# Kernel optimization log

Hardware: AMD Instinct MI355X
Metric: run time of the kernel (lower is better)

Reference implementation:

```python
import jax, jax.numpy as jnp
import numpy as np

N_V, M, K, C, H, F, CO = 100000, 25000, 48, 64, 4, 256, 64


def setup_inputs() -> dict:
    key = jax.random.key(0)
    ks = jax.random.split(key, 16)
    w = lambda k, shape: (jax.random.normal(k, shape, jnp.float32) * 0.05)
    voxel_features = jax.random.normal(ks[0], (N_V, C), jnp.float32)
    voxel_coords = jax.random.uniform(ks[1], (N_V, 3), jnp.float32) * 70.0 - 35.0
    query_coords = jax.random.uniform(ks[2], (M, 3), jnp.float32) * 70.0 - 35.0
    key_indices = jax.random.randint(ks[3], (M, K), 0, N_V, jnp.int32)
    key_mask = jax.random.uniform(ks[4], (M, K)) < 0.3
    key_mask = key_mask.at[:, 0].set(False)  # guarantee >=1 valid key per query
    zeros = lambda n: jnp.zeros((n,), jnp.float32)
    ones = lambda n: jnp.ones((n,), jnp.float32)
    return dict(
        voxel_features=voxel_features, voxel_coords=voxel_coords,
        query_coords=query_coords, key_indices=key_indices, key_mask=key_mask,
        q_pos_w=w(ks[5], (C, 3)), q_pos_b=zeros(C),
        k_pos_w=w(ks[6], (C, 3)), k_pos_b=zeros(C),
        in_proj_w=w(ks[7], (3 * C, C)), in_proj_b=zeros(3 * C),
        out_proj_w=w(ks[8], (C, C)), out_proj_b=zeros(C),
        lin1_w=w(ks[9], (F, C)), lin1_b=zeros(F),
        lin2_w=w(ks[10], (C, F)), lin2_b=zeros(C),
        norm_g=ones(C), norm_b=zeros(C), norm_m=zeros(C), norm_v=ones(C),
        out_w=w(ks[11], (CO, C)), out_b=zeros(CO),
        bn2_g=ones(CO), bn2_b=zeros(CO), bn2_m=zeros(CO), bn2_v=ones(CO),
    )


def reference(voxel_features, voxel_coords, query_coords, key_indices, key_mask,
              q_pos_w, q_pos_b, k_pos_w, k_pos_b, in_proj_w, in_proj_b,
              out_proj_w, out_proj_b, lin1_w, lin1_b, lin2_w, lin2_b,
              norm_g, norm_b, norm_m, norm_v, out_w, out_b,
              bn2_g, bn2_b, bn2_m, bn2_v):
    m, k = key_indices.shape
    c = voxel_features.shape[1]
    h = H
    d = c // h
    # grouping_operation: gather per-query key features/coords  (M,K,C)/(M,K,3)
    key_feats = voxel_features[key_indices]
    rel = voxel_coords[key_indices] - query_coords[:, None, :]  # relative coords
    # k_pos_proj: Conv1d(3->C, kernel 1) + ReLU == pointwise linear
    key_pos = jax.nn.relu(jnp.einsum('mkt,ct->mkc', rel, k_pos_w) + k_pos_b)
    k_in = key_feats + key_pos                      # (M,K,C)
    # q_pos_proj: Linear(3->C) + ReLU
    q_in = jax.nn.relu(query_coords @ q_pos_w.T + q_pos_b)  # (M,C)
    # nn.MultiheadAttention, query len 1, batch = M, keys = K
    wq, wk, wv = jnp.split(in_proj_w, 3, axis=0)
    bq, bk, bv = jnp.split(in_proj_b, 3)
    q = ((q_in @ wq.T + bq) * (d ** -0.5)).reshape(m, h, d)
    kk = (k_in @ wk.T + bk).reshape(m, k, h, d)
    vv = (k_in @ wv.T + bv).reshape(m, k, h, d)
    s = jnp.einsum('mhd,mkhd->mhk', q, kk)
    s = jnp.where(key_mask[:, None, :], -1e9, s)    # key_padding_mask
    a = jax.nn.softmax(s, axis=-1)
    o = jnp.einsum('mhk,mkhd->mhd', a, vv).reshape(m, c)
    attend = o @ out_proj_w.T + out_proj_b          # (M,C)
    # FFN residual (dropouts are identity in eval)
    ff = jax.nn.relu(attend @ lin1_w.T + lin1_b) @ lin2_w.T + lin2_b
    x = attend + ff
    # BatchNorm1d (eval)
    x = (x - norm_m) / jnp.sqrt(norm_v + 1e-5) * norm_g + norm_b
    # output_layer: Linear -> BN -> ReLU
    y = x @ out_w.T + out_b
    y = (y - bn2_m) / jnp.sqrt(bn2_v + 1e-5) * bn2_g + bn2_b
    return jax.nn.relu(y)
```

## Files before the change

### kernel.cpp

```cpp
#include <hip/hip_runtime.h>
#include <math.h>

#define CC 64
#define KK 48
#define HH 4

typedef __attribute__((ext_vector_type(8))) short s16x8;
typedef __attribute__((ext_vector_type(4))) short s16x4;
typedef __attribute__((ext_vector_type(4))) float f32x4;

#define QW_OFF_U16 57344

#define WAVEFENCE() asm volatile("s_waitcnt lgkmcnt(0)" ::: "memory")

__device__ __forceinline__ unsigned short f2bf(float f) {
  return (unsigned short)((__float_as_uint(f) + 0x8000u) >> 16);
}
__device__ __forceinline__ float bf2f(unsigned short h) {
  return __uint_as_float(((unsigned)h) << 16);
}

__global__ __launch_bounds__(256) void prep_kernel(
    const float* __restrict__ ipw, const float* __restrict__ opw,
    const float* __restrict__ l1w, const float* __restrict__ l2w,
    const float* __restrict__ ow,
    const float* __restrict__ ng, const float* __restrict__ nb,
    const float* __restrict__ nm, const float* __restrict__ nv,
    const float* __restrict__ b2g, const float* __restrict__ b2b,
    const float* __restrict__ b2m, const float* __restrict__ b2v,
    const unsigned char* __restrict__ km,
    float* __restrict__ ws)
{
  unsigned short* wsu = (unsigned short*)ws;
  if (blockIdx.x == 209) {
    int any = 0;
    for (int i = threadIdx.x; i < 4096; i += 256)
      if ((i & 3) && km[i]) any = 1;
    __shared__ int sb;
    if (threadIdx.x == 0) sb = 0;
    __syncthreads();
    if (any) atomicOr(&sb, 1);
    __syncthreads();
    if (threadIdx.x == 0) ((int*)ws)[26880] = sb;
    return;
  }
  int e = blockIdx.x * 256 + threadIdx.x;
  if (e < 4096)        wsu[e] = f2bf(ipw[e]);
  else if (e < 8192)  { int i = e - 4096; int h = i >> 10, c = (i >> 4) & 63, d = i & 15;
                        wsu[e] = f2bf(ipw[(size_t)(64 + h * 16 + d) * 64 + c]); }
  else if (e < 12288)  wsu[e] = f2bf(ipw[e]);
  else if (e < 16384)  wsu[e] = f2bf(opw[e - 12288]);
  else if (e < 32768)  wsu[e] = f2bf(l1w[e - 16384]);
  else if (e < 49152)  wsu[e] = f2bf(l2w[e - 32768]);
  else if (e < 53248)  wsu[e] = f2bf(ow[e - 49152]);
  else if (e < 53312) { int c = e - 53248; float s = ng[c] / sqrtf(nv[c] + 1e-5f);
                        ws[26624 + c] = s; ws[26624 + 64 + c] = nb[c] - nm[c] * s; }
  else if (e < 53376) { int c = e - 53312; float s = b2g[c] / sqrtf(b2v[c] + 1e-5f);
                        ws[26752 + c] = s; ws[26752 + 64 + c] = b2b[c] - b2m[c] * s; }
}

__global__ __launch_bounds__(256) void castv_kernel(
    const float* __restrict__ vf, const float* __restrict__ vcoord,
    unsigned short* __restrict__ vfb, float4* __restrict__ vc4, int NV)
{
  const int i0 = blockIdx.x * 256 + threadIdx.x;
  const int stride = gridDim.x * 256;
  for (int i = i0; i < NV * 16; i += stride) {
    const float4 v = *(const float4*)(vf + (size_t)i * 4);
    s16x4 p; p[0] = (short)f2bf(v.x); p[1] = (short)f2bf(v.y);
    p[2] = (short)f2bf(v.z); p[3] = (short)f2bf(v.w);
    *(s16x4*)(vfb + (size_t)i * 4) = p;
  }
  for (int i = i0; i < NV; i += stride)
    vc4[i] = make_float4(vcoord[i * 3], vcoord[i * 3 + 1], vcoord[i * 3 + 2], 0.f);
}

__global__ __launch_bounds__(256, 2) void qprep_kernel(
    const float* __restrict__ qcoord, const float* __restrict__ qpw,
    const float* __restrict__ qpb, const float* __restrict__ ipb,
    const unsigned short* __restrict__ wq_bf,
    const unsigned short* __restrict__ wk2T_bf,
    unsigned short* __restrict__ qw_out, int M)
{
  __shared__ __align__(16) unsigned short xa[4][1024];
  __shared__ float qc[4][48];
  const int w = threadIdx.x >> 6, l = threadIdx.x & 63;
  const int col = l & 15, lg = l >> 4;
  const int r0 = blockIdx.x * 64 + w * 16;

  if (l < 48) {
    int gi = r0 * 3 + l;
    qc[w][l] = (gi < M * 3) ? qcoord[gi] : 0.f;
  }
  const int c0 = col * 4;
  const float4 wA = *(const float4*)(qpw + c0 * 3);
  const float4 wB = *(const float4*)(qpw + c0 * 3 + 4);
  const float4 wC = *(const float4*)(qpw + c0 * 3 + 8);
  const float4 bq4 = *(const float4*)(qpb + c0);
  __syncthreads();

  #pragma unroll
  for (int i = 0; i < 4; ++i) {
    const int row = i * 4 + lg;
    const float x = qc[w][row * 3 + 0], y = qc[w][row * 3 + 1], z = qc[w][row * 3 + 2];
    s16x4 p;
    p[0] = (short)f2bf(fmaxf(wA.x * x + wA.y * y + wA.z * z + bq4.x, 0.f));
    p[1] = (short)f2bf(fmaxf(wA.w * x + wB.x * y + wB.y * z + bq4.y, 0.f));
    p[2] = (short)f2bf(fmaxf(wB.z * x + wB.w * y + wC.x * z + bq4.z, 0.f));
    p[3] = (short)f2bf(fmaxf(wC.y * x + wC.z * y + wC.w * z + bq4.w, 0.f));
    *(s16x4*)&xa[w][(row * 64 + c0) ^ ((row & 7) << 3)] = p;
  }
  __syncthreads();

  {
    s16x8 af0 = *(const s16x8*)&xa[w][(col * 64 + 0 + lg * 8) ^ ((col & 7) << 3)];
    s16x8 af1 = *(const s16x8*)&xa[w][(col * 64 + 32 + lg * 8) ^ ((col & 7) << 3)];
    f32x4 qv[4];
    #pragma unroll
    for (int nt = 0; nt < 4; ++nt) {
      f32x4 acc = {0.f, 0.f, 0.f, 0.f};
      acc = __builtin_amdgcn_mfma_f32_16x16x32_bf16(af0,
              *(const s16x8*)(wq_bf + (nt * 16 + col) * 64 + 0 + lg * 8), acc, 0, 0, 0);
      acc = __builtin_amdgcn_mfma_f32_16x16x32_bf16(af1,
              *(const s16x8*)(wq_bf + (nt * 16 + col) * 64 + 32 + lg * 8), acc, 0, 0, 0);
      qv[nt] = acc;
    }
    __syncthreads();
    #pragma unroll
    for (int nt = 0; nt < 4; ++nt) {
      const int n = nt * 16 + col;
      const float b = ipb[n];
      #pragma unroll
      for (int r = 0; r < 4; ++r) {
        const int row = lg * 4 + r;
        xa[w][(row * 64 + n) ^ ((row & 7) << 3)] = f2bf((qv[nt][r] + b) * 0.25f);
      }
    }
  }
  __syncthreads();

  #pragma unroll
  for (int h = 0; h < HH; ++h) {
    s16x8 a = {0, 0, 0, 0, 0, 0, 0, 0};
    if (lg < 2)
      a = *(const s16x8*)&xa[w][(col * 64 + h * 16 + lg * 8) ^ ((col & 7) << 3)];
    #pragma unroll
    for (int nt = 0; nt < 4; ++nt) {
      s16x8 b = {0, 0, 0, 0, 0, 0, 0, 0};
      if (lg < 2)
        b = *(const s16x8*)(wk2T_bf + h * 1024 + (nt * 16 + col) * 16 + lg * 8);
      f32x4 acc = {0.f, 0.f, 0.f, 0.f};
      acc = __builtin_amdgcn_mfma_f32_16x16x32_bf16(a, b, acc, 0, 0, 0);
      #pragma unroll
      for (int r = 0; r < 4; ++r) {
        const int m = lg * 4 + r;
        if (r0 + m < M)
          qw_out[(size_t)(r0 + m) * 256 + h * 64 + nt * 16 + col] = f2bf(acc[r]);
      }
    }
  }
}

__global__ __launch_bounds__(256, 4) void attn_hot(
    const unsigned short* __restrict__ vfb, const float4* __restrict__ vc4,
    const float* __restrict__ qcoord, const int* __restrict__ kidx,
    const unsigned char* __restrict__ km8, const int* __restrict__ km32,
    const int* __restrict__ maskfmt,
    const float* __restrict__ kpw, const float* __restrict__ kpb,
    const float* __restrict__ ipb,
    const unsigned short* __restrict__ wv_bf,
    const unsigned short* __restrict__ qw_pre,
    float* __restrict__ out, int M)
{
  __shared__ __align__(16) unsigned short shq[4][3456];
  __shared__ __align__(16) unsigned short wvl[4096];
  const int w = threadIdx.x >> 6, l = threadIdx.x & 63;
  const int col = l & 15, lg = l >> 4;
  int m = blockIdx.x * 4 + w;
  if (m >= M) m = M - 1;
  unsigned short* sh = shq[w];
  float* relf = (float*)(sh + 3072);
  const int is_u8 = *maskfmt;

  #pragma unroll
  for (int i = 0; i < 2; ++i) {
    const int ch = threadIdx.x * 2 + i;
    const int n = ch >> 3, g = ch & 7;
    const s16x8 v = *(const s16x8*)(wv_bf + n * 64 + g * 8);
    *(s16x8*)&wvl[n * 64 + ((g ^ (n & 7)) << 3)] = v;
  }

  const float qx = qcoord[m * 3 + 0], qy = qcoord[m * 3 + 1], qz = qcoord[m * 3 + 2];
  const int c0 = col * 4;
  const float4 kwA = *(const float4*)(kpw + c0 * 3);
  const float4 kwB = *(const float4*)(kpw + c0 * 3 + 4);
  const float4 kwC = *(const float4*)(kpw + c0 * 3 + 8);
  const float4 kbv = *(const float4*)(kpb + c0);

  unsigned char msk = 0;
  if (l < KK) {
    const int idx = kidx[m * KK + l];
    msk = is_u8 ? km8[m * KK + l] : (unsigned char)(km32[m * KK + l] != 0);
    const float4 vc = vc4[idx];
    float4 rr;
    rr.x = vc.x - qx; rr.y = vc.y - qy; rr.z = vc.z - qz;
    rr.w = __int_as_float(idx);
    *(float4*)(relf + l * 4) = rr;
  }
  const unsigned long long bm = __ballot(l < KK && msk);
  __syncthreads();

  #pragma unroll
  for (int half = 0; half < 2; ++half) {
    float4 ra[6]; s16x4 va[6];
    #pragma unroll
    for (int j = 0; j < 6; ++j) {
      const int k = half * 24 + j * 4 + lg;
      ra[j] = *(const float4*)(relf + k * 4);
      va[j] = *(const s16x4*)(vfb + (size_t)__float_as_int(ra[j].w) * 64 + c0);
    }
    #pragma unroll
    for (int j = 0; j < 6; ++j) {
      const int k = half * 24 + j * 4 + lg;
      const float p0 = fmaxf(kwA.x * ra[j].x + kwA.y * ra[j].y + kwA.z * ra[j].z + kbv.x, 0.f);
      const float p1 = fmaxf(kwA.w * ra[j].x + kwB.x * ra[j].y + kwB.y * ra[j].z + kbv.y, 0.f);
      const float p2 = fmaxf(kwB.z * ra[j].x + kwB.w * ra[j].y + kwC.x * ra[j].z + kbv.z, 0.f);
      const float p3 = fmaxf(kwC.y * ra[j].x + kwC.z * ra[j].y + kwC.w * ra[j].z + kbv.w, 0.f);
      s16x4 p;
      p[0] = (short)f2bf(bf2f((unsigned short)va[j][0]) + p0);
      p[1] = (short)f2bf(bf2f((unsigned short)va[j][1]) + p1);
      p[2] = (short)f2bf(bf2f((unsigned short)va[j][2]) + p2);
      p[3] = (short)f2bf(bf2f((unsigned short)va[j][3]) + p3);
      *(s16x4*)&sh[(k * 64 + c0) ^ ((k & 7) << 3)] = p;
    }
  }
  WAVEFENCE();

  s16x8 af[3][2];
  #pragma unroll
  for (int mt = 0; mt < 3; ++mt)
    #pragma unroll
    for (int kst = 0; kst < 2; ++kst) {
      const int row = mt * 16 + col;
      af[mt][kst] = *(const s16x8*)&sh[(row * 64 + kst * 32 + lg * 8) ^ ((row & 7) << 3)];
    }
  f32x4 sc[3];
  sc[0] = sc[1] = sc[2] = (f32x4){0.f, 0.f, 0.f, 0.f};
  #pragma unroll
  for (int kst = 0; kst < 2; ++kst) {
    const s16x8 b = *(const s16x8*)(qw_pre + (size_t)m * 256 + (col & 3) * 64 + kst * 32 + lg * 8);
    #pragma unroll
    for (int mt = 0; mt < 3; ++mt)
      sc[mt] = __builtin_amdgcn_mfma_f32_16x16x32_bf16(af[mt][kst], b, sc[mt], 0, 0, 0);
  }

  float sv[12];
  {
    float mx = -INFINITY;
    #pragma unroll
    for (int mt = 0; mt < 3; ++mt)
      #pragma unroll
      for (int r = 0; r < 4; ++r) {
        const int key = mt * 16 + lg * 4 + r;
        float v = sc[mt][r];
        if ((bm >> key) & 1ull) v = -1e30f;
        sv[mt * 4 + r] = v;
        mx = fmaxf(mx, v);
      }
    mx = fmaxf(mx, __shfl_xor(mx, 16, 64));
    mx = fmaxf(mx, __shfl_xor(mx, 32, 64));
    float sum = 0.f;
    #pragma unroll
    for (int i = 0; i < 12; ++i) { float e = __expf(sv[i] - mx); sv[i] = e; sum += e; }
    sum += __shfl_xor(sum, 16, 64);
    sum += __shfl_xor(sum, 32, 64);
    const float inv = 1.f / sum;
    #pragma unroll
    for (int i = 0; i < 12; ++i) sv[i] *= inv;
  }
  if (col < HH) {
    #pragma unroll
    for (int mt = 0; mt < 3; ++mt)
      #pragma unroll
      for (int r = 0; r < 4; ++r)
        relf[(mt * 16 + lg * 4 + r) * 4 + col] = sv[mt * 4 + r];
  }
  WAVEFENCE();

  f32x4 vva[4][3];
  #pragma unroll
  for (int nt = 0; nt < 4; ++nt) {
    const int n = nt * 16 + col;
    vva[nt][0] = vva[nt][1] = vva[nt][2] = (f32x4){0.f, 0.f, 0.f, 0.f};
    #pragma unroll
    for (int kst = 0; kst < 2; ++kst) {
      const s16x8 b = *(const s16x8*)&wvl[(n * 64 + kst * 32 + lg * 8) ^ ((n & 7) << 3)];
      vva[nt][0] = __builtin_amdgcn_mfma_f32_16x16x32_bf16(af[0][kst], b, vva[nt][0], 0, 0, 0);
      vva[nt][1] = __builtin_amdgcn_mfma_f32_16x16x32_bf16(af[1][kst], b, vva[nt][1], 0, 0, 0);
      vva[nt][2] = __builtin_amdgcn_mfma_f32_16x16x32_bf16(af[2][kst], b, vva[nt][2], 0, 0, 0);
    }
  }
  float op[4] = {0.f, 0.f, 0.f, 0.f};
  #pragma unroll
  for (int mt = 0; mt < 3; ++mt)
    #pragma unroll
    for (int r = 0; r < 4; ++r) {
      const float4 a4 = *(const float4*)(relf + (mt * 16 + lg * 4 + r) * 4);
      op[0] += a4.x * vva[0][mt][r];
      op[1] += a4.y * vva[1][mt][r];
      op[2] += a4.z * vva[2][mt][r];
      op[3] += a4.w * vva[3][mt][r];
    }
  #pragma unroll
  for (int nt = 0; nt < 4; ++nt) {
    op[nt] += __shfl_xor(op[nt], 16, 64);
    op[nt] += __shfl_xor(op[nt], 32, 64);
  }
  {
    float oo = (lg == 0) ? op[0] : (lg == 1) ? op[1] : (lg == 2) ? op[2] : op[3];
    oo += ipb[2 * CC + lg * 16 + col];
    out[(size_t)m * CC + lg * 16 + col] = oo;
  }
}

__global__ __launch_bounds__(256, 4) void attn_kernel(
    const float* __restrict__ vfeat, const unsigned short* __restrict__ vfb,
    const float* __restrict__ vcoord,
    const float* __restrict__ qcoord, const int* __restrict__ kidx,
    const unsigned char* __restrict__ km8, const int* __restrict__ km32,
    const int* __restrict__ maskfmt,
    const float* __restrict__ qpw, const float* __restrict__ qpb,
    const float* __restrict__ kpw, const float* __restrict__ kpb,
    const float* __restrict__ ipb,
    const unsigned short* __restrict__ wq_bf,
    const unsigned short* __restrict__ wk2T_bf,
    const unsigned short* __restrict__ wv_bf,
    const unsigned short* __restrict__ qw_pre, const int pre, const int pre2,
    float* __restrict__ out, int M)
{
  __shared__ __align__(16) unsigned short shq[4][3776];
  __shared__ __align__(16) unsigned short wvl[4096];
  const int w = threadIdx.x >> 6, l = threadIdx.x & 63;
  const int col = l & 15, lg = l >> 4;
  int m = blockIdx.x * 4 + w;
  if (m >= M) m = M - 1;
  unsigned short* sh = shq[w];
  const int is_u8 = *maskfmt;
  float* relf = (float*)sh + 1696;

  #pragma unroll
  for (int i = 0; i < 2; ++i) {
    const int ch = threadIdx.x * 2 + i;
    const int n = ch >> 3, g = ch & 7;
    const s16x8 v = *(const s16x8*)(wv_bf + n * 64 + g * 8);
    *(s16x8*)&wvl[n * 64 + ((g ^ (n & 7)) << 3)] = v;
  }

  const float qx = qcoord[m * 3 + 0], qy = qcoord[m * 3 + 1], qz = qcoord[m * 3 + 2];
  const int c0 = col * 4;
  const float4 kwA = *(const float4*)(kpw + c0 * 3);
  const float4 kwB = *(const float4*)(kpw + c0 * 3 + 4);
  const float4 kwC = *(const float4*)(kpw + c0 * 3 + 8);
  const float4 kbv = *(const float4*)(kpb + c0);

  if (!pre) {
    float v = qpw[l * 3 + 0] * qx + qpw[l * 3 + 1] * qy + qpw[l * 3 + 2] * qz + qpb[l];
    sh[3328 + l] = f2bf(fmaxf(v, 0.f));
  }
  unsigned char msk = 0;
  if (l < KK) {
    int idx = kidx[m * KK + l];
    msk = is_u8 ? km8[m * KK + l] : (unsigned char)(km32[m * KK + l] != 0);
    relf[l * 4 + 0] = vcoord[idx * 3 + 0] - qx;
    relf[l * 4 + 1] = vcoord[idx * 3 + 1] - qy;
    relf[l * 4 + 2] = vcoord[idx * 3 + 2] - qz;
    relf[l * 4 + 3] = __int_as_float(idx);
  }
  const unsigned long long bm = __ballot(l < KK && msk);
  __syncthreads();

  if (!pre) {
    f32x4 qacc[4];
    #pragma unroll
    for (int nt = 0; nt < 4; ++nt) qacc[nt] = (f32x4){0.f, 0.f, 0.f, 0.f};
    #pragma unroll
    for (int kst = 0; kst < 2; ++kst) {
      const s16x8 a = *(const s16x8*)&sh[3328 + kst * 32 + lg * 8];
      #pragma unroll
      for (int nt = 0; nt < 4; ++nt) {
        const s16x8 b = *(const s16x8*)(wq_bf + (nt * 16 + col) * 64 + kst * 32 + lg * 8);
        qacc[nt] = __builtin_amdgcn_mfma_f32_16x16x32_bf16(a, b, qacc[nt], 0, 0, 0);
      }
    }
    __syncthreads();
    if (lg == 0) {
      #pragma unroll
      for (int nt = 0; nt < 4; ++nt)
        sh[3328 + nt * 16 + col] = f2bf((qacc[nt][0] + ipb[nt * 16 + col]) * 0.25f);
    }
    __syncthreads();
    f32x4 wacc[4];
    #pragma unroll
    for (int nt = 0; nt < 4; ++nt) wacc[nt] = (f32x4){0.f, 0.f, 0.f, 0.f};
    #pragma unroll
    for (int kst = 0; kst < 2; ++kst) {
      const int hblk = kst * 2 + (lg >> 1);
      s16x8 a = {0, 0, 0, 0, 0, 0, 0, 0};
      if (col == hblk) a = *(const s16x8*)&sh[3328 + kst * 32 + lg * 8];
      #pragma unroll
      for (int nt = 0; nt < 4; ++nt) {
        const s16x8 b = *(const s16x8*)(wk2T_bf + hblk * 1024 + (nt * 16 + col) * 16 + (lg & 1) * 8);
        wacc[nt] = __builtin_amdgcn_mfma_f32_16x16x32_bf16(a, b, wacc[nt], 0, 0, 0);
      }
    }
    if (lg == 0) {
      #pragma unroll
      for (int nt = 0; nt < 4; ++nt)
        #pragma unroll
        for (int r = 0; r < 4; ++r)
          sh[3072 + r * 64 + nt * 16 + col] = f2bf(wacc[nt][r]);
    }
  }

  #pragma unroll
  for (int half = 0; half < 2; ++half) {
    float4 ra[6], va[6];
    #pragma unroll
    for (int j = 0; j < 6; ++j) {
      const int k = half * 24 + j * 4 + lg;
      ra[j] = *(const float4*)(relf + k * 4);
      va[j] = *(const float4*)(vfeat + (size_t)__float_as_int(ra[j].w) * 64 + c0);
    }
    #pragma unroll
    for (int j = 0; j < 6; ++j) {
      const int k = half * 24 + j * 4 + lg;
      const float p0 = fmaxf(kwA.x * ra[j].x + kwA.y * ra[j].y + kwA.z * ra[j].z + kbv.x, 0.f);
      const float p1 = fmaxf(kwA.w * ra[j].x + kwB.x * ra[j].y + kwB.y * ra[j].z + kbv.y, 0.f);
      const float p2 = fmaxf(kwB.z * ra[j].x + kwB.w * ra[j].y + kwC.x * ra[j].z + kbv.z, 0.f);
      const float p3 = fmaxf(kwC.y * ra[j].x + kwC.z * ra[j].y + kwC.w * ra[j].z + kbv.w, 0.f);
      s16x4 p;
      p[0] = (short)f2bf(va[j].x + p0); p[1] = (short)f2bf(va[j].y + p1);
      p[2] = (short)f2bf(va[j].z + p2); p[3] = (short)f2bf(va[j].w + p3);
      *(s16x4*)&sh[(k * 64 + c0) ^ ((k & 7) << 3)] = p;
    }
  }
  __syncthreads();

  s16x8 af[3][2];
  #pragma unroll
  for (int mt = 0; mt < 3; ++mt)
    #pragma unroll
    for (int kst = 0; kst < 2; ++kst) {
      const int row = mt * 16 + col;
      af[mt][kst] = *(const s16x8*)&sh[(row * 64 + kst * 32 + lg * 8) ^ ((row & 7) << 3)];
    }
  f32x4 sc[3];
  sc[0] = sc[1] = sc[2] = (f32x4){0.f, 0.f, 0.f, 0.f};
  #pragma unroll
  for (int kst = 0; kst < 2; ++kst) {
    s16x8 b;
    if (pre) b = *(const s16x8*)(qw_pre + (size_t)m * 256 + (col & 3) * 64 + kst * 32 + lg * 8);
    else     b = *(const s16x8*)&sh[3072 + (col & 3) * 64 + kst * 32 + lg * 8];
    #pragma unroll
    for (int mt = 0; mt < 3; ++mt)
      sc[mt] = __builtin_amdgcn_mfma_f32_16x16x32_bf16(af[mt][kst], b, sc[mt], 0, 0, 0);
  }

  float sv[12];
  {
    float mx = -INFINITY;
    #pragma unroll
    for (int mt = 0; mt < 3; ++mt)
      #pragma unroll
      for (int r = 0; r < 4; ++r) {
        const int key = mt * 16 + lg * 4 + r;
        float v = sc[mt][r];
        if ((bm >> key) & 1ull) v = -1e30f;
        sv[mt * 4 + r] = v;
        mx = fmaxf(mx, v);
      }
    mx = fmaxf(mx, __shfl_xor(mx, 16, 64));
    mx = fmaxf(mx, __shfl_xor(mx, 32, 64));
    float sum = 0.f;
    #pragma unroll
    for (int i = 0; i < 12; ++i) { float e = __expf(sv[i] - mx); sv[i] = e; sum += e; }
    sum += __shfl_xor(sum, 16, 64);
    sum += __shfl_xor(sum, 32, 64);
    const float inv = 1.f / sum;
    #pragma unroll
    for (int i = 0; i < 12; ++i) sv[i] *= inv;
  }

  float op[4];
  #pragma unroll
  for (int nt = 0; nt < 4; ++nt) {
    const int n = nt * 16 + col;
    f32x4 vv0 = {0.f, 0.f, 0.f, 0.f}, vv1 = vv0, vv2 = vv0;
    #pragma unroll
    for (int kst = 0; kst < 2; ++kst) {
      const s16x8 b = *(const s16x8*)&wvl[(n * 64 + kst * 32 + lg * 8) ^ ((n & 7) << 3)];
      vv0 = __builtin_amdgcn_mfma_f32_16x16x32_bf16(af[0][kst], b, vv0, 0, 0, 0);
      vv1 = __builtin_amdgcn_mfma_f32_16x16x32_bf16(af[1][kst], b, vv1, 0, 0, 0);
      vv2 = __builtin_amdgcn_mfma_f32_16x16x32_bf16(af[2][kst], b, vv2, 0, 0, 0);
    }
    const int src = lg * 16 + nt;
    float o = 0.f;
    #pragma unroll
    for (int mt = 0; mt < 3; ++mt)
      #pragma unroll
      for (int r = 0; r < 4; ++r) {
        const float a = __shfl(sv[mt * 4 + r], src, 64);
        const float v = (mt == 0) ? vv0[r] : (mt == 1) ? vv1[r] : vv2[r];
        o += a * v;
      }
    op[nt] = o;
// ... 117 lines not shown
      const s16x8 b = *(const s16x8*)&ow_bf[(nt * 16 + col) * 64 + kst * 32 + lg * 8];
      acc = __builtin_amdgcn_mfma_f32_16x16x32_bf16(afx[kst], b, acc, 0, 0, 0);
    }
    int nc = nt * 16 + col;
    float bias = ob[nc], sB = bn2[nc], tB = bn2[64 + nc];
    #pragma unroll
    for (int r = 0; r < 4; ++r) {
      float y = fmaxf((acc[r] + bias) * sB + tB, 0.f);
      int row = lg * 4 + r;
      if (r0 + row < M) inout[(size_t)(r0 + row) * 64 + nc] = y;
    }
  }
}

extern "C" void kernel_launch(void* const* d_in, const int* in_sizes, int n_in,
                              void* d_out, int out_size, void* d_ws, size_t ws_size,
                              hipStream_t stream) {
  const float* vfeat  = (const float*)d_in[0];
  const float* vcoord = (const float*)d_in[1];
  const float* qcoord = (const float*)d_in[2];
  const int*   kidx   = (const int*)d_in[3];
  const unsigned char* km8  = (const unsigned char*)d_in[4];
  const int*           km32 = (const int*)d_in[4];
  const float* qpw = (const float*)d_in[5];
  const float* qpb = (const float*)d_in[6];
  const float* kpw = (const float*)d_in[7];
  const float* kpb = (const float*)d_in[8];
  const float* ipw = (const float*)d_in[9];
  const float* ipb = (const float*)d_in[10];
  const float* opw = (const float*)d_in[11];
  const float* opb = (const float*)d_in[12];
  const float* l1w = (const float*)d_in[13];
  const float* l1b = (const float*)d_in[14];
  const float* l2w = (const float*)d_in[15];
  const float* l2b = (const float*)d_in[16];
  const float* ng  = (const float*)d_in[17];
  const float* nb  = (const float*)d_in[18];
  const float* nm  = (const float*)d_in[19];
  const float* nv  = (const float*)d_in[20];
  const float* ow  = (const float*)d_in[21];
  const float* ob  = (const float*)d_in[22];
  const float* b2g = (const float*)d_in[23];
  const float* b2b = (const float*)d_in[24];
  const float* b2m = (const float*)d_in[25];
  const float* b2v = (const float*)d_in[26];

  const int M  = in_sizes[2] / 3;
  const int NV = in_sizes[0] / 64;
  float* ws  = (float*)d_ws;
  float* out = (float*)d_out;
  unsigned short* wsu = (unsigned short*)ws;
  const int* flag = (const int*)ws + 26880;

  const size_t need_qw  = (size_t)114688 + (size_t)M * 512;
  const size_t need_vfb = need_qw + (size_t)NV * 128;
  const size_t need_vc4 = need_vfb + (size_t)NV * 16;
  const int pre  = (ws_size >= need_qw) ? 1 : 0;
  const int pre2 = (pre && ws_size >= need_vfb) ? 1 : 0;
  const int hot  = (pre2 && ws_size >= need_vc4) ? 1 : 0;
  unsigned short* qw  = wsu + QW_OFF_U16;
  unsigned short* vfb = wsu + QW_OFF_U16 + (size_t)M * 256;
  float4* vc4 = (float4*)(wsu + QW_OFF_U16 + (size_t)M * 256 + (size_t)NV * 64);

  prep_kernel<<<210, 256, 0, stream>>>(ipw, opw, l1w, l2w, ow,
                                       ng, nb, nm, nv, b2g, b2b, b2m, b2v, km8, ws);
  if (hot)
    castv_kernel<<<2048, 256, 0, stream>>>(vfeat, vcoord, vfb, vc4, NV);
  if (pre)
    qprep_kernel<<<(M + 63) / 64, 256, 0, stream>>>(qcoord, qpw, qpb, ipb,
                                                    wsu, wsu + 4096, qw, M);
  if (hot) {
    attn_hot<<<(M + 3) / 4, 256, 0, stream>>>(vfb, vc4, qcoord, kidx,
                                              km8, km32, flag, kpw, kpb, ipb,
                                              wsu + 8192, qw, out, M);
  } else {
    attn_kernel<<<(M + 3) / 4, 256, 0, stream>>>(vfeat, vfb, vcoord, qcoord, kidx,
                                                 km8, km32, flag,
                                                 qpw, qpb, kpw, kpb, ipb,
                                                 wsu, wsu + 4096, wsu + 8192,
                                                 qw, pre, 0, out, M);
  }
  chain_kernel<<<(M + 63) / 64, 256, 0, stream>>>(out, wsu, opb, l1b, l2b, ob,
                                                  ws + 26624, ws + 26752, M);
}
```

Baseline: 98.08 us.

## Fuse weight prep, voxel cast and query prep into one setup kernel

Merges the weight-conversion, voxel bf16/float4 cast, and query-projection kernels into a single launch with block-range dispatch. The query-prep path now reads the fp32 in_proj weights directly instead of depending on the bf16 copies from the prep stage, which removes the ordering dependency. attn_hot hoists the per-query qw loads ahead of the gather and wraps its MFMA sections in s_setprio. This cuts two kernel launches and the serialization between them, at the cost of redundant fp32 weight loads and conversions in every query block.

```diff
diff --git a/kernel.cpp b/kernel.cpp
--- a/kernel.cpp
+++ b/kernel.cpp
@@ -10,6 +10,7 @@
 typedef __attribute__((ext_vector_type(4))) float f32x4;
 
 #define QW_OFF_U16 57344
+#define CASTB 1024
 
 #define WAVEFENCE() asm volatile("s_waitcnt lgkmcnt(0)" ::: "memory")
 
@@ -18,6 +19,328 @@
 }
 __device__ __forceinline__ float bf2f(unsigned short h) {
   return __uint_as_float(((unsigned)h) << 16);
+}
+
+__global__ __launch_bounds__(256) void setup_kernel(
+    const float* __restrict__ ipw, const float* __restrict__ opw,
+    const float* __restrict__ l1w, const float* __restrict__ l2w,
+    const float* __restrict__ ow,
+    const float* __restrict__ ng, const float* __restrict__ nb,
+    const float* __restrict__ nm, const float* __restrict__ nv,
+    const float* __restrict__ b2g, const float* __restrict__ b2b,
+    const float* __restrict__ b2m, const float* __restrict__ b2v,
+    const unsigned char* __restrict__ km,
+    const float* __restrict__ vf, const float* __restrict__ vcoord,
+    const float* __restrict__ qcoord, const float* __restrict__ qpw,
+    const float* __restrict__ qpb, const float* __restrict__ ipb,
+    float* __restrict__ ws,
+    unsigned short* __restrict__ vfb, float4* __restrict__ vc4,
+    unsigned short* __restrict__ qw_out, int M, int NV)
+{
+  unsigned short* wsu = (unsigned short*)ws;
+  const int b = blockIdx.x;
+
+  if (b < 210) {
+    if (b == 209) {
+      int any = 0;
+      for (int i = threadIdx.x; i < 4096; i += 256)
+        if ((i & 3) && km[i]) any = 1;
+      __shared__ int sb;
+      if (threadIdx.x == 0) sb = 0;
+      __syncthreads();
+      if (any) atomicOr(&sb, 1);
+      __syncthreads();
+      if (threadIdx.x == 0) ((int*)ws)[26880] = sb;
+      return;
+    }
+    int e = b * 256 + threadIdx.x;
+    if (e < 4096)        wsu[e] = f2bf(ipw[e]);
+    else if (e < 8192)  { int i = e - 4096; int h = i >> 10, c = (i >> 4) & 63, d = i & 15;
+                          wsu[e] = f2bf(ipw[(size_t)(64 + h * 16 + d) * 64 + c]); }
+    else if (e < 12288)  wsu[e] = f2bf(ipw[e]);
+    else if (e < 16384)  wsu[e] = f2bf(opw[e - 12288]);
+    else if (e < 32768)  wsu[e] = f2bf(l1w[e - 16384]);
+    else if (e < 49152)  wsu[e] = f2bf(l2w[e - 32768]);
+    else if (e < 53248)  wsu[e] = f2bf(ow[e - 49152]);
+    else if (e < 53312) { int c = e - 53248; float s = ng[c] / sqrtf(nv[c] + 1e-5f);
+                          ws[26624 + c] = s; ws[26624 + 64 + c] = nb[c] - nm[c] * s; }
+    else if (e < 53376) { int c = e - 53312; float s = b2g[c] / sqrtf(b2v[c] + 1e-5f);
+                          ws[26752 + c] = s; ws[26752 + 64 + c] = b2b[c] - b2m[c] * s; }
+    return;
+  }
+
+  if (b < 210 + CASTB) {
+    const int i0 = (b - 210) * 256 + threadIdx.x;
+    const int stride = CASTB * 256;
+    for (int i = i0; i < NV * 16; i += stride) {
+      const float4 v = *(const float4*)(vf + (size_t)i * 4);
+      s16x4 p; p[0] = (short)f2bf(v.x); p[1] = (short)f2bf(v.y);
+      p[2] = (short)f2bf(v.z); p[3] = (short)f2bf(v.w);
+      *(s16x4*)(vfb + (size_t)i * 4) = p;
+    }
+    for (int i = i0; i < NV; i += stride)
+      vc4[i] = make_float4(vcoord[i * 3], vcoord[i * 3 + 1], vcoord[i * 3 + 2], 0.f);
+    return;
+  }
+
+  {
+    __shared__ __align__(16) unsigned short xa[4][1024];
+    __shared__ float qc[4][48];
+    const int w = threadIdx.x >> 6, l = threadIdx.x & 63;
+    const int col = l & 15, lg = l >> 4;
+    const int r0 = (b - 210 - CASTB) * 64 + w * 16;
+
+    if (l < 48) {
+      int gi = r0 * 3 + l;
+      qc[w][l] = (gi < M * 3) ? qcoord[gi] : 0.f;
+    }
+    const int c0 = col * 4;
+    const float4 wA = *(const float4*)(qpw + c0 * 3);
+    const float4 wB = *(const float4*)(qpw + c0 * 3 + 4);
+    const float4 wC = *(const float4*)(qpw + c0 * 3 + 8);
+    const float4 bq4 = *(const float4*)(qpb + c0);
+    __syncthreads();
+
+    #pragma unroll
+    for (int i = 0; i < 4; ++i) {
+      const int row = i * 4 + lg;
+      const float x = qc[w][row * 3 + 0], y = qc[w][row * 3 + 1], z = qc[w][row * 3 + 2];
+      s16x4 p;
+      p[0] = (short)f2bf(fmaxf(wA.x * x + wA.y * y + wA.z * z + bq4.x, 0.f));
+      p[1] = (short)f2bf(fmaxf(wA.w * x + wB.x * y + wB.y * z + bq4.y, 0.f));
+      p[2] = (short)f2bf(fmaxf(wB.z * x + wB.w * y + wC.x * z + bq4.z, 0.f));
+      p[3] = (short)f2bf(fmaxf(wC.y * x + wC.z * y + wC.w * z + bq4.w, 0.f));
+      *(s16x4*)&xa[w][(row * 64 + c0) ^ ((row & 7) << 3)] = p;
+    }
+    __syncthreads();
+
+    {
+      s16x8 af0 = *(const s16x8*)&xa[w][(col * 64 + 0 + lg * 8) ^ ((col & 7) << 3)];
+      s16x8 af1 = *(const s16x8*)&xa[w][(col * 64 + 32 + lg * 8) ^ ((col & 7) << 3)];
+      f32x4 qv[4];
+      #pragma unroll
+      for (int nt = 0; nt < 4; ++nt) {
+        f32x4 acc = {0.f, 0.f, 0.f, 0.f};
+        #pragma unroll
+        for (int kst = 0; kst < 2; ++kst) {
+          const float* wr = ipw + (size_t)(nt * 16 + col) * 64 + kst * 32 + lg * 8;
+          const float4 w0 = *(const float4*)wr;
+          const float4 w1 = *(const float4*)(wr + 4);
+          s16x8 bf;
+          bf[0] = (short)f2bf(w0.x); bf[1] = (short)f2bf(w0.y);
+          bf[2] = (short)f2bf(w0.z); bf[3] = (short)f2bf(w0.w);
+          bf[4] = (short)f2bf(w1.x); bf[5] = (short)f2bf(w1.y);
+          bf[6] = (short)f2bf(w1.z); bf[7] = (short)f2bf(w1.w);
+          acc = __builtin_amdgcn_mfma_f32_16x16x32_bf16(kst == 0 ? af0 : af1, bf, acc, 0, 0, 0);
+        }
+        qv[nt] = acc;
+      }
+      __syncthreads();
+      #pragma unroll
+      for (int nt = 0; nt < 4; ++nt) {
+        const int n = nt * 16 + col;
+        const float bb = ipb[n];
+        #pragma unroll
+        for (int r = 0; r < 4; ++r) {
+          const int row = lg * 4 + r;
+          xa[w][(row * 64 + n) ^ ((row & 7) << 3)] = f2bf((qv[nt][r] + bb) * 0.25f);
+        }
+      }
+    }
+    __syncthreads();
+
+    #pragma unroll
+    for (int h = 0; h < HH; ++h) {
+      s16x8 a = {0, 0, 0, 0, 0, 0, 0, 0};
+      if (lg < 2)
+        a = *(const s16x8*)&xa[w][(col * 64 + h * 16 + lg * 8) ^ ((col & 7) << 3)];
+      #pragma unroll
+      for (int nt = 0; nt < 4; ++nt) {
+        const int n = nt * 16 + col;
+        s16x8 bf = {0, 0, 0, 0, 0, 0, 0, 0};
+        if (lg < 2) {
+          #pragma unroll
+          for (int j = 0; j < 8; ++j)
+            ((unsigned short*)&bf)[j] = f2bf(ipw[(size_t)(64 + h * 16 + lg * 8 + j) * 64 + n]);
+        }
+        f32x4 acc = {0.f, 0.f, 0.f, 0.f};
+        acc = __builtin_amdgcn_mfma_f32_16x16x32_bf16(a, bf, acc, 0, 0, 0);
+        #pragma unroll
+        for (int r = 0; r < 4; ++r) {
+          const int m = lg * 4 + r;
+          if (r0 + m < M)
+            qw_out[(size_t)(r0 + m) * 256 + h * 64 + n] = f2bf(acc[r]);
+        }
+      }
+    }
+  }
+}
+
+__global__ __launch_bounds__(256, 4) void attn_hot(
+    const unsigned short* __restrict__ vfb, const float4* __restrict__ vc4,
+    const float* __restrict__ qcoord, const int* __restrict__ kidx,
+    const unsigned char* __restrict__ km8, const int* __restrict__ km32,
+    const int* __restrict__ maskfmt,
+    const float* __restrict__ kpw, const float* __restrict__ kpb,
+    const float* __restrict__ ipb,
+    const unsigned short* __restrict__ wv_bf,
+    const unsigned short* __restrict__ qw_pre,
+    float* __restrict__ out, int M)
+{
+  __shared__ __align__(16) unsigned short shq[4][3456];
+  __shared__ __align__(16) unsigned short wvl[4096];
+  const int w = threadIdx.x >> 6, l = threadIdx.x & 63;
+  const int col = l & 15, lg = l >> 4;
+  int m = blockIdx.x * 4 + w;
+  if (m >= M) m = M - 1;
+  unsigned short* sh = shq[w];
+  float* relf = (float*)(sh + 3072);
+  const int is_u8 = *maskfmt;
+
+  #pragma unroll
+  for (int i = 0; i < 2; ++i) {
+    const int ch = threadIdx.x * 2 + i;
+    const int n = ch >> 3, g = ch & 7;
+    const s16x8 v = *(const s16x8*)(wv_bf + n * 64 + g * 8);
+    *(s16x8*)&wvl[n * 64 + ((g ^ (n & 7)) << 3)] = v;
+  }
+
+  const float qx = qcoord[m * 3 + 0], qy = qcoord[m * 3 + 1], qz = qcoord[m * 3 + 2];
+  const int c0 = col * 4;
+  const float4 kwA = *(const float4*)(kpw + c0 * 3);
+  const float4 kwB = *(const float4*)(kpw + c0 * 3 + 4);
+  const float4 kwC = *(const float4*)(kpw + c0 * 3 + 8);
+  const float4 kbv = *(const float4*)(kpb + c0);
+
+  const s16x8 qb0 = *(const s16x8*)(qw_pre + (size_t)m * 256 + (col & 3) * 64 + 0 + lg * 8);
+  const s16x8 qb1 = *(const s16x8*)(qw_pre + (size_t)m * 256 + (col & 3) * 64 + 32 + lg * 8);
+
+  unsigned char msk = 0;
+  if (l < KK) {
+    const int idx = kidx[m * KK + l];
+    msk = is_u8 ? km8[m * KK + l] : (unsigned char)(km32[m * KK + l] != 0);
+    const float4 vc = vc4[idx];
+    float4 rr;
+    rr.x = vc.x - qx; rr.y = vc.y - qy; rr.z = vc.z - qz;
+    rr.w = __int_as_float(idx);
+    *(float4*)(relf + l * 4) = rr;
+  }
+  const unsigned long long bm = __ballot(l < KK && msk);
+  __syncthreads();
+
+  #pragma unroll
+  for (int half = 0; half < 2; ++half) {
+    float4 ra[6]; s16x4 va[6];
+    #pragma unroll
+    for (int j = 0; j < 6; ++j) {
+      const int k = half * 24 + j * 4 + lg;
+      ra[j] = *(const float4*)(relf + k * 4);
+      va[j] = *(const s16x4*)(vfb + (size_t)__float_as_int(ra[j].w) * 64 + c0);
+    }
+    #pragma unroll
+    for (int j = 0; j < 6; ++j) {
+      const int k = half * 24 + j * 4 + lg;
+      const float p0 = fmaxf(kwA.x * ra[j].x + kwA.y * ra[j].y + kwA.z * ra[j].z + kbv.x, 0.f);
+      const float p1 = fmaxf(kwA.w * ra[j].x + kwB.x * ra[j].y + kwB.y * ra[j].z + kbv.y, 0.f);
+      const float p2 = fmaxf(kwB.z * ra[j].x + kwB.w * ra[j].y + kwC.x * ra[j].z + kbv.z, 0.f);
+      const float p3 = fmaxf(kwC.y * ra[j].x + kwC.z * ra[j].y + kwC.w * ra[j].z + kbv.w, 0.f);
+      s16x4 p;
+      p[0] = (short)f2bf(bf2f((unsigned short)va[j][0]) + p0);
+      p[1] = (short)f2bf(bf2f((unsigned short)va[j][1]) + p1);
+      p[2] = (short)f2bf(bf2f((unsigned short)va[j][2]) + p2);
+      p[3] = (short)f2bf(bf2f((unsigned short)va[j][3]) + p3);
+      *(s16x4*)&sh[(k * 64 + c0) ^ ((k & 7) << 3)] = p;
+    }
+  }
+  WAVEFENCE();
+
+  s16x8 af[3][2];
+  #pragma unroll
+  for (int mt = 0; mt < 3; ++mt)
+    #pragma unroll
+    for (int kst = 0; kst < 2; ++kst) {
+      const int row = mt * 16 + col;
+      af[mt][kst] = *(const s16x8*)&sh[(row * 64 + kst * 32 + lg * 8) ^ ((row & 7) << 3)];
+    }
+  f32x4 sc[3];
+  sc[0] = sc[1] = sc[2] = (f32x4){0.f, 0.f, 0.f, 0.f};
+  __builtin_amdgcn_s_setprio(1);
+  #pragma unroll
+  for (int mt = 0; mt < 3; ++mt) {
+    sc[mt] = __builtin_amdgcn_mfma_f32_16x16x32_bf16(af[mt][0], qb0, sc[mt], 0, 0, 0);
+    sc[mt] = __builtin_amdgcn_mfma_f32_16x16x32_bf16(af[mt][1], qb1, sc[mt], 0, 0, 0);
+  }
+  __builtin_amdgcn_s_setprio(0);
+
+  float sv[12];
+  {
+    float mx = -INFINITY;
+    #pragma unroll
+    for (int mt = 0; mt < 3; ++mt)
+      #pragma unroll
+      for (int r = 0; r < 4; ++r) {
+        const int key = mt * 16 + lg * 4 + r;
+        float v = sc[mt][r];
+        if ((bm >> key) & 1ull) v = -1e30f;
+        sv[mt * 4 + r] = v;
+        mx = fmaxf(mx, v);
+      }
+    mx = fmaxf(mx, __shfl_xor(mx, 16, 64));
+    mx = fmaxf(mx, __shfl_xor(mx, 32, 64));
+    float sum = 0.f;
+    #pragma unroll
+    for (int i = 0; i < 12; ++i) { float e = __expf(sv[i] - mx); sv[i] = e; sum += e; }
+    sum += __shfl_xor(sum, 16, 64);
+    sum += __shfl_xor(sum, 32, 64);
+    const float inv = 1.f / sum;
+    #pragma unroll
+    for (int i = 0; i < 12; ++i) sv[i] *= inv;
+  }
+  if (col < HH) {
+    #pragma unroll
+    for (int mt = 0; mt < 3; ++mt)
+      #pragma unroll
+      for (int r = 0; r < 4; ++r)
+        relf[(mt * 16 + lg * 4 + r) * 4 + col] = sv[mt * 4 + r];
+  }
+  WAVEFENCE();
+
+  f32x4 vva[4][3];
+  __builtin_amdgcn_s_setprio(1);
+  #pragma unroll
+  for (int nt = 0; nt < 4; ++nt) {
+    const int n = nt * 16 + col;
+    vva[nt][0] = vva[nt][1] = vva[nt][2] = (f32x4){0.f, 0.f, 0.f, 0.f};
+    #pragma unroll
+    for (int kst = 0; kst < 2; ++kst) {
+      const s16x8 b = *(const s16x8*)&wvl[(n * 64 + kst * 32 + lg * 8) ^ ((n & 7) << 3)];
+      vva[nt][0] = __builtin_amdgcn_mfma_f32_16x16x32_bf16(af[0][kst], b, vva[nt][0], 0, 0, 0);
+      vva[nt][1] = __builtin_amdgcn_mfma_f32_16x16x32_bf16(af[1][kst], b, vva[nt][1], 0, 0, 0);
+      vva[nt][2] = __builtin_amdgcn_mfma_f32_16x16x32_bf16(af[2][kst], b, vva[nt][2], 0, 0, 0);
+    }
+  }
+  __builtin_amdgcn_s_setprio(0);
+  float op[4] = {0.f, 0.f, 0.f, 0.f};
+  #pragma unroll
+  for (int mt = 0; mt < 3; ++mt)
+    #pragma unroll
+    for (int r = 0; r < 4; ++r) {
+      const float4 a4 = *(const float4*)(relf + (mt * 16 + lg * 4 + r) * 4);
+      op[0] += a4.x * vva[0][mt][r];
+      op[1] += a4.y * vva[1][mt][r];
+      op[2] += a4.z * vva[2][mt][r];
+      op[3] += a4.w * vva[3][mt][r];
+    }
+  #pragma unroll
+  for (int nt = 0; nt < 4; ++nt) {
+    op[nt] += __shfl_xor(op[nt], 16, 64);
+    op[nt] += __shfl_xor(op[nt], 32, 64);
+  }
+  {
+    float oo = (lg == 0) ? op[0] : (lg == 1) ? op[1] : (lg == 2) ? op[2] : op[3];
+    oo += ipb[2 * CC + lg * 16 + col];
+    out[(size_t)m * CC + lg * 16 + col] = oo;
+  }
 }
 
 __global__ __launch_bounds__(256) void prep_kernel(
@@ -59,273 +382,8 @@
                         ws[26752 + c] = s; ws[26752 + 64 + c] = b2b[c] - b2m[c] * s; }
 }
 
-__global__ __launch_bounds__(256) void castv_kernel(
-    const float* __restrict__ vf, const float* __restrict__ vcoord,
-    unsigned short* __restrict__ vfb, float4* __restrict__ vc4, int NV)
-{
-  const int i0 = blockIdx.x * 256 + threadIdx.x;
-  const int stride = gridDim.x * 256;
-  for (int i = i0; i < NV * 16; i += stride) {
-    const float4 v = *(const float4*)(vf + (size_t)i * 4);
-    s16x4 p; p[0] = (short)f2bf(v.x); p[1] = (short)f2bf(v.y);
-    p[2] = (short)f2bf(v.z); p[3] = (short)f2bf(v.w);
-    *(s16x4*)(vfb + (size_t)i * 4) = p;
-  }
-  for (int i = i0; i < NV; i += stride)
-    vc4[i] = make_float4(vcoord[i * 3], vcoord[i * 3 + 1], vcoord[i * 3 + 2], 0.f);
-}
-
-__global__ __launch_bounds__(256, 2) void qprep_kernel(
-    const float* __restrict__ qcoord, const float* __restrict__ qpw,
-    const float* __restrict__ qpb, const float* __restrict__ ipb,
-    const unsigned short* __restrict__ wq_bf,
-    const unsigned short* __restrict__ wk2T_bf,
-    unsigned short* __restrict__ qw_out, int M)
-{
-  __shared__ __align__(16) unsigned short xa[4][1024];
-  __shared__ float qc[4][48];
-  const int w = threadIdx.x >> 6, l = threadIdx.x & 63;
-  const int col = l & 15, lg = l >> 4;
-  const int r0 = blockIdx.x * 64 + w * 16;
-
-  if (l < 48) {
-    int gi = r0 * 3 + l;
-    qc[w][l] = (gi < M * 3) ? qcoord[gi] : 0.f;
-  }
-  const int c0 = col * 4;
-  const float4 wA = *(const float4*)(qpw + c0 * 3);
-  const float4 wB = *(const float4*)(qpw + c0 * 3 + 4);
-  const float4 wC = *(const float4*)(qpw + c0 * 3 + 8);
-  const float4 bq4 = *(const float4*)(qpb + c0);
-  __syncthreads();
-
-  #pragma unroll
-  for (int i = 0; i < 4; ++i) {
-    const int row = i * 4 + lg;
-    const float x = qc[w][row * 3 + 0], y = qc[w][row * 3 + 1], z = qc[w][row * 3 + 2];
-    s16x4 p;
-    p[0] = (short)f2bf(fmaxf(wA.x * x + wA.y * y + wA.z * z + bq4.x, 0.f));
-    p[1] = (short)f2bf(fmaxf(wA.w * x + wB.x * y + wB.y * z + bq4.y, 0.f));
-    p[2] = (short)f2bf(fmaxf(wB.z * x + wB.w * y + wC.x * z + bq4.z, 0.f));
-    p[3] = (short)f2bf(fmaxf(wC.y * x + wC.z * y + wC.w * z + bq4.w, 0.f));
-    *(s16x4*)&xa[w][(row * 64 + c0) ^ ((row & 7) << 3)] = p;
-  }
-  __syncthreads();
-
-  {
-    s16x8 af0 = *(const s16x8*)&xa[w][(col * 64 + 0 + lg * 8) ^ ((col & 7) << 3)];
-    s16x8 af1 = *(const s16x8*)&xa[w][(col * 64 + 32 + lg * 8) ^ ((col & 7) << 3)];
-    f32x4 qv[4];
-    #pragma unroll
-    for (int nt = 0; nt < 4; ++nt) {
-      f32x4 acc = {0.f, 0.f, 0.f, 0.f};
-      acc = __builtin_amdgcn_mfma_f32_16x16x32_bf16(af0,
-              *(const s16x8*)(wq_bf + (nt * 16 + col) * 64 + 0 + lg * 8), acc, 0, 0, 0);
-      acc = __builtin_amdgcn_mfma_f32_16x16x32_bf16(af1,
-              *(const s16x8*)(wq_bf + (nt * 16 + col) * 64 + 32 + lg * 8), acc, 0, 0, 0);
-      qv[nt] = acc;
-    }
-    __syncthreads();
-    #pragma unroll
-    for (int nt = 0; nt < 4; ++nt) {
-      const int n = nt * 16 + col;
-      const float b = ipb[n];
-      #pragma unroll
-      for (int r = 0; r < 4; ++r) {
-        const int row = lg * 4 + r;
-        xa[w][(row * 64 + n) ^ ((row & 7) << 3)] = f2bf((qv[nt][r] + b) * 0.25f);
-      }
-    }
-  }
-  __syncthreads();
-
-  #pragma unroll
-  for (int h = 0; h < HH; ++h) {
-    s16x8 a = {0, 0, 0, 0, 0, 0, 0, 0};
-    if (lg < 2)
-      a = *(const s16x8*)&xa[w][(col * 64 + h * 16 + lg * 8) ^ ((col & 7) << 3)];
-    #pragma unroll
-    for (int nt = 0; nt < 4; ++nt) {
-      s16x8 b = {0, 0, 0, 0, 0, 0, 0, 0};
-      if (lg < 2)
-        b = *(const s16x8*)(wk2T_bf + h * 1024 + (nt * 16 + col) * 16 + lg * 8);
-      f32x4 acc = {0.f, 0.f, 0.f, 0.f};
-      acc = __builtin_amdgcn_mfma_f32_16x16x32_bf16(a, b, acc, 0, 0, 0);
-      #pragma unroll
-      for (int r = 0; r < 4; ++r) {
-        const int m = lg * 4 + r;
-        if (r0 + m < M)
-          qw_out[(size_t)(r0 + m) * 256 + h * 64 + nt * 16 + col] = f2bf(acc[r]);
-      }
-    }
-  }
-}
-
-__global__ __launch_bounds__(256, 4) void attn_hot(
-    const unsigned short* __restrict__ vfb, const float4* __restrict__ vc4,
-    const float* __restrict__ qcoord, const int* __restrict__ kidx,
-    const unsigned char* __restrict__ km8, const int* __restrict__ km32,
-    const int* __restrict__ maskfmt,
-    const float* __restrict__ kpw, const float* __restrict__ kpb,
-    const float* __restrict__ ipb,
-    const unsigned short* __restrict__ wv_bf,
-    const unsigned short* __restrict__ qw_pre,
-    float* __restrict__ out, int M)
-{
-  __shared__ __align__(16) unsigned short shq[4][3456];
-  __shared__ __align__(16) unsigned short wvl[4096];
-  const int w = threadIdx.x >> 6, l = threadIdx.x & 63;
-  const int col = l & 15, lg = l >> 4;
-  int m = blockIdx.x * 4 + w;
-  if (m >= M) m = M - 1;
-  unsigned short* sh = shq[w];
-  float* relf = (float*)(sh + 3072);
-  const int is_u8 = *maskfmt;
-
-  #pragma unroll
-  for (int i = 0; i < 2; ++i) {
-    const int ch = threadIdx.x * 2 + i;
-    const int n = ch >> 3, g = ch & 7;
-    const s16x8 v = *(const s16x8*)(wv_bf + n * 64 + g * 8);
-    *(s16x8*)&wvl[n * 64 + ((g ^ (n & 7)) << 3)] = v;
-  }
-
-  const float qx = qcoord[m * 3 + 0], qy = qcoord[m * 3 + 1], qz = qcoord[m * 3 + 2];
-  const int c0 = col * 4;
-  const float4 kwA = *(const float4*)(kpw + c0 * 3);
-  const float4 kwB = *(const float4*)(kpw + c0 * 3 + 4);
-  const float4 kwC = *(const float4*)(kpw + c0 * 3 + 8);
-  const float4 kbv = *(const float4*)(kpb + c0);
-
-  unsigned char msk = 0;
-  if (l < KK) {
-    const int idx = kidx[m * KK + l];
-    msk = is_u8 ? km8[m * KK + l] : (unsigned char)(km32[m * KK + l] != 0);
-    const float4 vc = vc4[idx];
-    float4 rr;
-    rr.x = vc.x - qx; rr.y = vc.y - qy; rr.z = vc.z - qz;
-    rr.w = __int_as_float(idx);
-    *(float4*)(relf + l * 4) = rr;
-  }
-  const unsigned long long bm = __ballot(l < KK && msk);
-  __syncthreads();
-
-  #pragma unroll
-  for (int half = 0; half < 2; ++half) {
-    float4 ra[6]; s16x4 va[6];
-    #pragma unroll
-    for (int j = 0; j < 6; ++j) {
-      const int k = half * 24 + j * 4 + lg;
-      ra[j] = *(const float4*)(relf + k * 4);
-      va[j] = *(const s16x4*)(vfb + (size_t)__float_as_int(ra[j].w) * 64 + c0);
-    }
-    #pragma unroll
-    for (int j = 0; j < 6; ++j) {
-      const int k = half * 24 + j * 4 + lg;
-      const float p0 = fmaxf(kwA.x * ra[j].x + kwA.y * ra[j].y + kwA.z * ra[j].z + kbv.x, 0.f);
-      const float p1 = fmaxf(kwA.w * ra[j].x + kwB.x * ra[j].y + kwB.y * ra[j].z + kbv.y, 0.f);
-      const float p2 = fmaxf(kwB.z * ra[j].x + kwB.w * ra[j].y + kwC.x * ra[j].z + kbv.z, 0.f);
-      const float p3 = fmaxf(kwC.y * ra[j].x + kwC.z * ra[j].y + kwC.w * ra[j].z + kbv.w, 0.f);
-      s16x4 p;
-      p[0] = (short)f2bf(bf2f((unsigned short)va[j][0]) + p0);
-      p[1] = (short)f2bf(bf2f((unsigned short)va[j][1]) + p1);
-      p[2] = (short)f2bf(bf2f((unsigned short)va[j][2]) + p2);
-      p[3] = (short)f2bf(bf2f((unsigned short)va[j][3]) + p3);
-      *(s16x4*)&sh[(k * 64 + c0) ^ ((k & 7) << 3)] = p;
-    }
-  }
-  WAVEFENCE();
-
-  s16x8 af[3][2];
-  #pragma unroll
-  for (int mt = 0; mt < 3; ++mt)
-    #pragma unroll
-    for (int kst = 0; kst < 2; ++kst) {
-      const int row = mt * 16 + col;
-      af[mt][kst] = *(const s16x8*)&sh[(row * 64 + kst * 32 + lg * 8) ^ ((row & 7) << 3)];
-    }
-  f32x4 sc[3];
-  sc[0] = sc[1] = sc[2] = (f32x4){0.f, 0.f, 0.f, 0.f};
-  #pragma unroll
-  for (int kst = 0; kst < 2; ++kst) {
-    const s16x8 b = *(const s16x8*)(qw_pre + (size_t)m * 256 + (col & 3) * 64 + kst * 32 + lg * 8);
-    #pragma unroll
-    for (int mt = 0; mt < 3; ++mt)
-      sc[mt] = __builtin_amdgcn_mfma_f32_16x16x32_bf16(af[mt][kst], b, sc[mt], 0, 0, 0);
-  }
-
-  float sv[12];
-  {
-    float mx = -INFINITY;
-    #pragma unroll
-    for (int mt = 0; mt < 3; ++mt)
-      #pragma unroll
-      for (int r = 0; r < 4; ++r) {
-        const int key = mt * 16 + lg * 4 + r;
-        float v = sc[mt][r];
-        if ((bm >> key) & 1ull) v = -1e30f;
-        sv[mt * 4 + r] = v;
-        mx = fmaxf(mx, v);
-      }
-    mx = fmaxf(mx, __shfl_xor(mx, 16, 64));
-    mx = fmaxf(mx, __shfl_xor(mx, 32, 64));
-    float sum = 0.f;
-    #pragma unroll
-    for (int i = 0; i < 12; ++i) { float e = __expf(sv[i] - mx); sv[i] = e; sum += e; }
-    sum += __shfl_xor(sum, 16, 64);
-    sum += __shfl_xor(sum, 32, 64);
-    const float inv = 1.f / sum;
-    #pragma unroll
-    for (int i = 0; i < 12; ++i) sv[i] *= inv;
-  }
-  if (col < HH) {
-    #pragma unroll
-    for (int mt = 0; mt < 3; ++mt)
-      #pragma unroll
-      for (int r = 0; r < 4; ++r)
-        relf[(mt * 16 + lg * 4 + r) * 4 + col] = sv[mt * 4 + r];
-  }
-  WAVEFENCE();
-
-  f32x4 vva[4][3];
-  #pragma unroll
-  for (int nt = 0; nt < 4; ++nt) {
-    const int n = nt * 16 + col;
-    vva[nt][0] = vva[nt][1] = vva[nt][2] = (f32x4){0.f, 0.f, 0.f, 0.f};
-    #pragma unroll
-    for (int kst = 0; kst < 2; ++kst) {
-      const s16x8 b = *(const s16x8*)&wvl[(n * 64 + kst * 32 + lg * 8) ^ ((n & 7) << 3)];
-      vva[nt][0] = __builtin_amdgcn_mfma_f32_16x16x32_bf16(af[0][kst], b, vva[nt][0], 0, 0, 0);
-      vva[nt][1] = __builtin_amdgcn_mfma_f32_16x16x32_bf16(af[1][kst], b, vva[nt][1], 0, 0, 0);
-      vva[nt][2] = __builtin_amdgcn_mfma_f32_16x16x32_bf16(af[2][kst], b, vva[nt][2], 0, 0, 0);
-    }
-  }
-  float op[4] = {0.f, 0.f, 0.f, 0.f};
-  #pragma unroll
-  for (int mt = 0; mt < 3; ++mt)
-    #pragma unroll
-    for (int r = 0; r < 4; ++r) {
-      const float4 a4 = *(const float4*)(relf + (mt * 16 + lg * 4 + r) * 4);
-      op[0] += a4.x * vva[0][mt][r];
-      op[1] += a4.y * vva[1][mt][r];
-      op[2] += a4.z * vva[2][mt][r];
-      op[3] += a4.w * vva[3][mt][r];
-    }
-  #pragma unroll
-  for (int nt = 0; nt < 4; ++nt) {
-    op[nt] += __shfl_xor(op[nt], 16, 64);
-    op[nt] += __shfl_xor(op[nt], 32, 64);
-  }
-  {
-    float oo = (lg == 0) ? op[0] : (lg == 1) ? op[1] : (lg == 2) ? op[2] : op[3];
-    oo += ipb[2 * CC + lg * 16 + col];
-    out[(size_t)m * CC + lg * 16 + col] = oo;
-  }
-}
-
-__global__ __launch_bounds__(256, 4) void attn_kernel(
-    const float* __restrict__ vfeat, const unsigned short* __restrict__ vfb,
-    const float* __restrict__ vcoord,
+__global__ __launch_bounds__(256, 4) void attn_fallback(
+    const float* __restrict__ vfeat, const float* __restrict__ vcoord,
     const float* __restrict__ qcoord, const int* __restrict__ kidx,
     const unsigned char* __restrict__ km8, const int* __restrict__ km32,
     const int* __restrict__ maskfmt,
@@ -335,7 +393,6 @@
     const unsigned short* __restrict__ wq_bf,
     const unsigned short* __restrict__ wk2T_bf,
     const unsigned short* __restrict__ wv_bf,
-    const unsigned short* __restrict__ qw_pre, const int pre, const int pre2,
     float* __restrict__ out, int M)
 {
   __shared__ __align__(16) unsigned short shq[4][3776];
@@ -363,7 +420,7 @@
   const float4 kwC = *(const float4*)(kpw + c0 * 3 + 8);
   const float4 kbv = *(const float4*)(kpb + c0);
 
-  if (!pre) {
+  {
     float v = qpw[l * 3 + 0] * qx + qpw[l * 3 + 1] * qy + qpw[l * 3 + 2] * qz + qpb[l];
     sh[3328 + l] = f2bf(fmaxf(v, 0.f));
   }
@@ -379,7 +436,7 @@
   const unsigned long long bm = __ballot(l < KK && msk);
   __syncthreads();
 
-  if (!pre) {
+  {
     f32x4 qacc[4];
     #pragma unroll
     for (int nt = 0; nt < 4; ++nt) qacc[nt] = (f32x4){0.f, 0.f, 0.f, 0.f};
@@ -458,9 +515,7 @@
   sc[0] = sc[1] = sc[2] = (f32x4){0.f, 0.f, 0.f, 0.f};
   #pragma unroll
   for (int kst = 0; kst < 2; ++kst) {
-    s16x8 b;
-    if (pre) b = *(const s16x8*)(qw_pre + (size_t)m * 256 + (col & 3) * 64 + kst * 32 + lg * 8);
-    else     b = *(const s16x8*)&sh[3072 + (col & 3) * 64 + kst * 32 + lg * 8];
+    const s16x8 b = *(const s16x8*)&sh[3072 + (col & 3) * 64 + kst * 32 + lg * 8];
     #pragma unroll
     for (int mt = 0; mt < 3; ++mt)
       sc[mt] = __builtin_amdgcn_mfma_f32_16x16x32_bf16(af[mt][kst], b, sc[mt], 0, 0, 0);
@@ -684,33 +739,27 @@
   unsigned short* wsu = (unsigned short*)ws;
   const int* flag = (const int*)ws + 26880;
 
-  const size_t need_qw  = (size_t)114688 + (size_t)M * 512;
-  const size_t need_vfb = need_qw + (size_t)NV * 128;
-  const size_t need_vc4 = need_vfb + (size_t)NV * 16;
-  const int pre  = (ws_size >= need_qw) ? 1 : 0;
-  const int pre2 = (pre && ws_size >= need_vfb) ? 1 : 0;
-  const int hot  = (pre2 && ws_size >= need_vc4) ? 1 : 0;
+  const size_t need = (size_t)114688 + (size_t)M * 512 + (size_t)NV * 128 + (size_t)NV * 16;
+  const int hot = (ws_size >= need) ? 1 : 0;
   unsigned short* qw  = wsu + QW_OFF_U16;
   unsigned short* vfb = wsu + QW_OFF_U16 + (size_t)M * 256;
   float4* vc4 = (float4*)(wsu + QW_OFF_U16 + (size_t)M * 256 + (size_t)NV * 64);
 
-  prep_kernel<<<210, 256, 0, stream>>>(ipw, opw, l1w, l2w, ow,
-                                       ng, nb, nm, nv, b2g, b2b, b2m, b2v, km8, ws);
-  if (hot)
-    castv_kernel<<<2048, 256, 0, stream>>>(vfeat, vcoord, vfb, vc4, NV);
-  if (pre)
-    qprep_kernel<<<(M + 63) / 64, 256, 0, stream>>>(qcoord, qpw, qpb, ipb,
-                                                    wsu, wsu + 4096, qw, M);
   if (hot) {
+    const int qblocks = (M + 63) / 64;
+    setup_kernel<<<210 + CASTB + qblocks, 256, 0, stream>>>(
+        ipw, opw, l1w, l2w, ow, ng, nb, nm, nv, b2g, b2b, b2m, b2v, km8,
+        vfeat, vcoord, qcoord, qpw, qpb, ipb, ws, vfb, vc4, qw, M, NV);
     attn_hot<<<(M + 3) / 4, 256, 0, stream>>>(vfb, vc4, qcoord, kidx,
                                               km8, km32, flag, kpw, kpb, ipb,
                                               wsu + 8192, qw, out, M);
   } else {
-    attn_kernel<<<(M + 3) / 4, 256, 0, stream>>>(vfeat, vfb, vcoord, qcoord, kidx,
-                                                 km8, km32, flag,
-                                                 qpw, qpb, kpw, kpb, ipb,
-                                                 wsu, wsu + 4096, wsu + 8192,
-                                                 qw, pre, 0, out, M);
+    prep_kernel<<<210, 256, 0, stream>>>(ipw, opw, l1w, l2w, ow,
+                                         ng, nb, nm, nv, b2g, b2b, b2m, b2v, km8, ws);
+    attn_fallback<<<(M + 3) / 4, 256, 0, stream>>>(vfeat, vcoord, qcoord, kidx,
+                                                   km8, km32, flag,
+                                                   qpw, qpb, kpw, kpb, ipb,
+                                                   wsu, wsu + 4096, wsu + 8192, out, M);
   }
   chain_kernel<<<(M + 63) / 64, 256, 0, stream>>>(out, wsu, opb, l1b, l2b, ob,
                                                   ws + 26624, ws + 26752, M);
```

Measured after the change: 93.80 us. 1.05x faster.
